# Kernel tuning notes

Hardware: AMD Instinct MI355X
Metric: run time of the kernel (lower is better)

Reference implementation:

```python
import jax, jax.numpy as jnp
import numpy as np

N, E, CIN, H, OUT, L = 100000, 1200000, 3, 64, 3, 3
EPS = 1e-7  # GENConv message epsilon


def setup_inputs() -> dict:
    key = jax.random.key(0)
    ks = jax.random.split(key, 8)
    f = lambda k, s, sc=0.1: (jax.random.normal(k, s, jnp.float32) * sc)
    return {
        "x": f(ks[0], (N, CIN), 1.0),
        "edge_index": jax.random.randint(ks[1], (2, E), 0, N, jnp.int32),
        "enc_W": f(ks[2], (CIN, H)),
        "enc_b": jnp.zeros((H,), jnp.float32),
        "t": jnp.ones((L,), jnp.float32),
        "mlp_W1": f(ks[3], (L, H, 2 * H)),
        "mlp_b1": jnp.zeros((L, 2 * H), jnp.float32),
        "mlp_g": jnp.ones((L, 2 * H), jnp.float32),
        "mlp_beta": jnp.zeros((L, 2 * H), jnp.float32),
        "mlp_W2": f(ks[4], (L, 2 * H, H)),
        "mlp_b2": jnp.zeros((L, H), jnp.float32),
        "ln_g": jnp.ones((L, H), jnp.float32),
        "ln_b": jnp.zeros((L, H), jnp.float32),
        "lin_W": f(ks[5], (H, OUT)),
        "lin_b": jnp.zeros((OUT,), jnp.float32),
    }


def layer_norm(x, g, b, eps=1e-5):
    mu = jnp.mean(x, -1, keepdims=True)
    var = jnp.var(x, -1, keepdims=True)
    return (x - mu) * jax.lax.rsqrt(var + eps) * g + b


def genconv(x, src, dst, t, W1, b1, g, beta, W2, b2):
    # message: relu(x_j) + eps, per edge  [E, H]
    msg = jax.nn.relu(x[src]) + EPS
    # softmax aggregation with temperature t (per-destination, elementwise)
    logits = msg * t
    m = jax.ops.segment_max(logits, dst, num_segments=N)            # [N, H]
    w = jnp.exp(logits - m[dst])                                    # [E, H]
    denom = jax.ops.segment_sum(w, dst, num_segments=N)             # [N, H]
    agg = jax.ops.segment_sum(msg * (w / denom[dst]), dst, num_segments=N)
    # root residual + MLP [H -> 2H -> LN -> ReLU -> H]
    out = agg + x
    h = jax.nn.relu(layer_norm(out @ W1 + b1, g, beta))
    return h @ W2 + b2


def reference(x, edge_index, enc_W, enc_b, t, mlp_W1, mlp_b1, mlp_g, mlp_beta,
              mlp_W2, mlp_b2, ln_g, ln_b, lin_W, lin_b):
    src, dst = edge_index[0], edge_index[1]
    h = x @ enc_W + enc_b
    # layers[0].conv applied directly (DeepGCN 'res+' convention)
    h = genconv(h, src, dst, t[0], mlp_W1[0], mlp_b1[0], mlp_g[0], mlp_beta[0],
                mlp_W2[0], mlp_b2[0])
    for i in range(1, L):
        z = jax.nn.relu(layer_norm(h, ln_g[i], ln_b[i]))
        h = h + genconv(z, src, dst, t[i], mlp_W1[i], mlp_b1[i], mlp_g[i],
                        mlp_beta[i], mlp_W2[i], mlp_b2[i])
    h = jax.nn.relu(layer_norm(h, ln_g[0], ln_b[0]))
    return h @ lin_W + lin_b
```

## Files before the change

### kernel.cpp

```cpp
#include <hip/hip_runtime.h>
#include <hip/hip_bf16.h>
#include <math.h>

#define H 64
#define H2 128
#define EPS_MSG 1e-7f
#define LN_EPS 1e-5f
#define LOG2E 1.4426950408889634f
#define LN2 0.6931471805599453f
#define YSTR 136
#define BSTRIDE 4608
#define OSTRIDE 5376
#define CHUNK 8192

typedef __attribute__((ext_vector_type(8))) short bf16x8;
typedef __attribute__((ext_vector_type(4))) float f32x4;

__device__ __forceinline__ unsigned short f2bf(float f) {
    union { float f; unsigned int i; } x; x.f = f;
    unsigned int r = x.i + 0x7FFF + ((x.i >> 16) & 1);
    return (unsigned short)(r >> 16);
}

__global__ __launch_bounds__(256) void bscat_k(const int* __restrict__ src,
                                               const int* __restrict__ dst,
                                               int* __restrict__ bcnt,
                                               unsigned int* __restrict__ bdata,
                                               int E, int nbuck) {
    __shared__ int h[512], base[512];
    for (int i = threadIdx.x; i < nbuck; i += 256) h[i] = 0;
    __syncthreads();
    int lo = blockIdx.x * CHUNK;
    int hi = lo + CHUNK; if (hi > E) hi = E;
    for (int i = lo + threadIdx.x; i < hi; i += 256)
        atomicAdd(&h[dst[i] >> 8], 1);
    __syncthreads();
    for (int i = threadIdx.x; i < nbuck; i += 256) {
        int c = h[i];
        base[i] = c ? atomicAdd(&bcnt[i], c) : 0;
        h[i] = 0;
    }
    __syncthreads();
    for (int i = lo + threadIdx.x; i < hi; i += 256) {
        int d = dst[i];
        int b = d >> 8;
        int pos = base[b] + atomicAdd(&h[b], 1);
        bdata[(size_t)b * BSTRIDE + pos] = ((unsigned int)src[i] << 8) | (unsigned int)(d & 255);
    }
}

__global__ __launch_bounds__(256) void bsort_k(const unsigned int* __restrict__ bdata,
                                               const int* __restrict__ bcnt,
                                               int* __restrict__ row_beg, int* __restrict__ row_end,
                                               int* __restrict__ srcs_sorted,
                                               int Nn) {
    __shared__ unsigned int stage[BSTRIDE];
    __shared__ int cnt[256], pre[256], ex[256];
    int b = blockIdx.x, tid = threadIdx.x;
    int m = bcnt[b]; if (m > BSTRIDE) m = BSTRIDE;
    size_t lo = (size_t)b * BSTRIDE;
    int oLo = b * OSTRIDE;
    for (int i = tid; i < m; i += 256) stage[i] = bdata[lo + i];
    cnt[tid] = 0;
    __syncthreads();
    for (int i = tid; i < m; i += 256) atomicAdd(&cnt[stage[i] & 255], 1);
    __syncthreads();
    int myc = cnt[tid];
    int pc = (myc + 3) & ~3;
    pre[tid] = pc;
    __syncthreads();
    #pragma unroll
    for (int off = 1; off < 256; off <<= 1) {
        int t = (tid >= off) ? pre[tid - off] : 0;
        __syncthreads();
        pre[tid] += t;
        __syncthreads();
    }
    int pexcl = pre[tid] - pc;
    ex[tid] = pexcl;
    int node = (b << 8) + tid;
    if (node < Nn) {
        row_beg[node] = oLo + pexcl;
        row_end[node] = oLo + pexcl + pc;
    }
    for (int p = myc; p < pc; ++p) srcs_sorted[oLo + pexcl + p] = Nn;
    __syncthreads();
    cnt[tid] = 0;
    __syncthreads();
    for (int i = tid; i < m; i += 256) {
        unsigned int v = stage[i];
        int dl = v & 255;
        int p = ex[dl] + atomicAdd(&cnt[dl], 1);
        srcs_sorted[oLo + p] = (int)(v >> 8);
    }
}

__global__ void wprep_k(const float* __restrict__ W1, const float* __restrict__ W2,
                        unsigned short* __restrict__ Wf1, unsigned short* __restrict__ Wf2) {
    int idx = blockIdx.x * 256 + threadIdx.x;
    const int half = 3 * 8192;
    if (idx < half) {
        int layer = idx / 8192, rem = idx - layer * 8192;
        int t = rem >> 9;
        int l = (rem >> 3) & 63;
        int i = rem & 7;
        int h = t >> 3, ct = t & 7;
        int kpos = h * 32 + (l >> 4) * 8 + i;
        int k = (kpos & 3) * 16 + (kpos >> 2);
        int j = ct * 16 + (l & 15);
        Wf1[idx] = f2bf(W1[(size_t)layer * H * H2 + (size_t)k * H2 + j]);
    } else if (idx < 2 * half) {
        int id2 = idx - half;
        int layer = id2 / 8192, rem = id2 - layer * 8192;
        int t = rem >> 9;
        int l = (rem >> 3) & 63;
        int i = rem & 7;
        int kk = t >> 2, ct2 = t & 3;
        int k = kk * 32 + (l >> 4) * 8 + i;
        int j = ct2 * 16 + (l & 15);
        Wf2[id2] = f2bf(W2[(size_t)layer * H2 * H + (size_t)k * H + j]);
    }
}

__global__ void encoder_k(const float* __restrict__ x, const float* __restrict__ W,
                          const float* __restrict__ b,
                          unsigned short* __restrict__ Zself, unsigned short* __restrict__ Zmsg,
                          const float* __restrict__ t, int Nn) {
    int idx = blockIdx.x * blockDim.x + threadIdx.x;
    if (idx >= (Nn + 1) * H) return;
    int n = idx >> 6, c = idx & 63;
    if (n == Nn) { Zmsg[idx] = f2bf(-200.f); return; }
    float acc = b[c];
    #pragma unroll
    for (int k = 0; k < 3; ++k) acc = fmaf(x[n * 3 + k], W[k * H + c], acc);
    int j = (c & 15) * 4 + (c >> 4);
    Zself[(size_t)n * H + j] = f2bf(acc);
    Zmsg[(size_t)n * H + j]  = f2bf(fmaxf(acc, 0.f) * (LOG2E) * t[0]);
}

__global__ __launch_bounds__(256) void gather_k(
    const unsigned short* __restrict__ Zmsg, const unsigned short* __restrict__ Zself,
    unsigned short* __restrict__ Gbf,
    const int* __restrict__ row_beg, const int* __restrict__ row_end,
    const int* __restrict__ srcs,
    const float* __restrict__ t, int layer, int Nn)
{
    int wid = threadIdx.x >> 6, lane = threadIdx.x & 63;
    int nA = blockIdx.x * 8 + wid * 2;
    if (nA >= Nn) return;
    int nB = nA + 1;
    bool hasB = (nB < Nn);
    int slot = lane >> 4;
    int ch4  = lane & 15;
    float scale = (LN2) * __builtin_amdgcn_rcpf(t[layer]);

    int begA = row_beg[nA];
    int itA  = (row_end[nA] - begA) >> 2;
    int begB = hasB ? row_beg[nB] : begA;
    int itB  = hasB ? (row_end[nB] - begB) >> 2 : 0;
    const int* spA = srcs + begA;
    const int* spB = srcs + begB;

    const unsigned short* selfTab = (layer == 0) ? Zself : Zmsg;
    uint2 svA = *(const uint2*)(selfTab + (size_t)nA * H + ch4 * 4);
    uint2 svB = hasB ? *(const uint2*)(selfTab + (size_t)nB * H + ch4 * 4) : svA;

    #define LQ(qq, sp, i)                                                      \
        {                                                                      \
            int s = sp[4 * (i) + slot];                                        \
            qq = *(const uint2*)(Zmsg + (size_t)s * H + ch4 * 4);              \
        }

    #define PROC(qq, d0, d1, d2, d3, s0, s1, s2, s3)                           \
        {                                                                      \
            float u0 = __uint_as_float(qq.x << 16);                            \
            float u1 = __uint_as_float(qq.x & 0xffff0000u);                    \
            float u2 = __uint_as_float(qq.y << 16);                            \
            float u3 = __uint_as_float(qq.y & 0xffff0000u);                    \
            float w0 = __builtin_amdgcn_exp2f(u0);                             \
            float w1 = __builtin_amdgcn_exp2f(u1);                             \
            float w2 = __builtin_amdgcn_exp2f(u2);                             \
            float w3 = __builtin_amdgcn_exp2f(u3);                             \
            d0 += w0; d1 += w1; d2 += w2; d3 += w3;                            \
            s0 = fmaf(u0, w0, s0); s1 = fmaf(u1, w1, s1);                      \
            s2 = fmaf(u2, w2, s2); s3 = fmaf(u3, w3, s3);                      \
        }
    #define PROCA(qq) PROC(qq, dA0, dA1, dA2, dA3, sA0, sA1, sA2, sA3)
    #define PROCB(qq) PROC(qq, dB0, dB1, dB2, dB3, sB0, sB1, sB2, sB3)

    uint2 a0 = {0,0}, a1 = {0,0}, a2 = {0,0}, a3 = {0,0};
    uint2 b0 = {0,0}, b1 = {0,0}, b2 = {0,0}, b3 = {0,0};
    if (itA > 0) LQ(a0, spA, 0)
    if (itB > 0) LQ(b0, spB, 0)
    if (itA > 1) LQ(a1, spA, 1)
    if (itB > 1) LQ(b1, spB, 1)
    if (itA > 2) LQ(a2, spA, 2)
    if (itB > 2) LQ(b2, spB, 2)
    if (itA > 3) LQ(a3, spA, 3)
    if (itB > 3) LQ(b3, spB, 3)

    float dA0=0.f,dA1=0.f,dA2=0.f,dA3=0.f,sA0=0.f,sA1=0.f,sA2=0.f,sA3=0.f;
    float dB0=0.f,dB1=0.f,dB2=0.f,dB3=0.f,sB0=0.f,sB1=0.f,sB2=0.f,sB3=0.f;

    if (itA > 0) {
        int i = 0;
        #pragma unroll 1
        for (; i + 4 < itA; i += 4) {
            PROCA(a0) LQ(a0, spA, i + 4)
            PROCA(a1) if (i + 5 < itA) LQ(a1, spA, i + 5)
            PROCA(a2) if (i + 6 < itA) LQ(a2, spA, i + 6)
            PROCA(a3) if (i + 7 < itA) LQ(a3, spA, i + 7)
        }
        PROCA(a0)
        if (i + 1 < itA) PROCA(a1)
        if (i + 2 < itA) PROCA(a2)
        if (i + 3 < itA) PROCA(a3)
    }
    if (itB > 0) {
        int i = 0;
        #pragma unroll 1
        for (; i + 4 < itB; i += 4) {
            PROCB(b0) LQ(b0, spB, i + 4)
            PROCB(b1) if (i + 5 < itB) LQ(b1, spB, i + 5)
            PROCB(b2) if (i + 6 < itB) LQ(b2, spB, i + 6)
            PROCB(b3) if (i + 7 < itB) LQ(b3, spB, i + 7)
        }
        PROCB(b0)
        if (i + 1 < itB) PROCB(b1)
        if (i + 2 < itB) PROCB(b2)
        if (i + 3 < itB) PROCB(b3)
    }
    #undef LQ
    #undef PROC
    #undef PROCA
    #undef PROCB

    #pragma unroll
    for (int o = 16; o <= 32; o <<= 1) {
        dA0 += __shfl_xor(dA0, o, 64); dA1 += __shfl_xor(dA1, o, 64);
        dA2 += __shfl_xor(dA2, o, 64); dA3 += __shfl_xor(dA3, o, 64);
        sA0 += __shfl_xor(sA0, o, 64); sA1 += __shfl_xor(sA1, o, 64);
        sA2 += __shfl_xor(sA2, o, 64); sA3 += __shfl_xor(sA3, o, 64);
        dB0 += __shfl_xor(dB0, o, 64); dB1 += __shfl_xor(dB1, o, 64);
        dB2 += __shfl_xor(dB2, o, 64); dB3 += __shfl_xor(dB3, o, 64);
        sB0 += __shfl_xor(sB0, o, 64); sB1 += __shfl_xor(sB1, o, 64);
        sB2 += __shfl_xor(sB2, o, 64); sB3 += __shfl_xor(sB3, o, 64);
    }

    if (slot == 0) {
        {
            float o0 = __uint_as_float(svA.x << 16);
            float o1 = __uint_as_float(svA.x & 0xffff0000u);
            float o2 = __uint_as_float(svA.y << 16);
            float o3 = __uint_as_float(svA.y & 0xffff0000u);
            if (layer != 0) { o0 *= scale; o1 *= scale; o2 *= scale; o3 *= scale; }
            if (itA > 0) {
                o0 += fmaf(sA0 * __builtin_amdgcn_rcpf(dA0), scale, EPS_MSG);
                o1 += fmaf(sA1 * __builtin_amdgcn_rcpf(dA1), scale, EPS_MSG);
                o2 += fmaf(sA2 * __builtin_amdgcn_rcpf(dA2), scale, EPS_MSG);
                o3 += fmaf(sA3 * __builtin_amdgcn_rcpf(dA3), scale, EPS_MSG);
            }
            uint2 pv;
            pv.x = (unsigned int)f2bf(o0) | ((unsigned int)f2bf(o1) << 16);
            pv.y = (unsigned int)f2bf(o2) | ((unsigned int)f2bf(o3) << 16);
            *(uint2*)(Gbf + (size_t)nA * H + ch4 * 4) = pv;
        }
        if (hasB) {
            float o0 = __uint_as_float(svB.x << 16);
            float o1 = __uint_as_float(svB.x & 0xffff0000u);
            float o2 = __uint_as_float(svB.y << 16);
            float o3 = __uint_as_float(svB.y & 0xffff0000u);
            if (layer != 0) { o0 *= scale; o1 *= scale; o2 *= scale; o3 *= scale; }
            if (itB > 0) {
                o0 += fmaf(sB0 * __builtin_amdgcn_rcpf(dB0), scale, EPS_MSG);
                o1 += fmaf(sB1 * __builtin_amdgcn_rcpf(dB1), scale, EPS_MSG);
                o2 += fmaf(sB2 * __builtin_amdgcn_rcpf(dB2), scale, EPS_MSG);
                o3 += fmaf(sB3 * __builtin_amdgcn_rcpf(dB3), scale, EPS_MSG);
            }
            uint2 pv;
            pv.x = (unsigned int)f2bf(o0) | ((unsigned int)f2bf(o1) << 16);
            pv.y = (unsigned int)f2bf(o2) | ((unsigned int)f2bf(o3) << 16);
            *(uint2*)(Gbf + (size_t)nB * H + ch4 * 4) = pv;
        }
    }
}

__global__ __launch_bounds__(256) void mlp_k(
    const unsigned short* __restrict__ Gbf, float* __restrict__ B,
    const unsigned short* __restrict__ Wf1, const unsigned short* __restrict__ Wf2,
    const float* __restrict__ b1, const float* __restrict__ g,
    const float* __restrict__ beta, const float* __restrict__ b2,
    unsigned short* __restrict__ Zmsg,
    const float* __restrict__ tptr, const float* __restrict__ ln_g,
    const float* __restrict__ ln_b, const float* __restrict__ lin_W,
    const float* __restrict__ lin_b, float* __restrict__ outp,
    int wlayer, int lnidx, int resid, int mode, int Nn)
{
    __shared__ __align__(16) unsigned short yt[4][16 * YSTR];
    int wid = threadIdx.x >> 6, lane = threadIdx.x & 63;
    int gq = lane >> 4, c = lane & 15;
    int n0 = (blockIdx.x * 4 + wid) * 16;

    Wf1 += (size_t)wlayer * 8192; Wf2 += (size_t)wlayer * 8192;
    b1 += wlayer * H2; g += wlayer * H2; beta += wlayer * H2; b2 += wlayer * H;

    int nA = n0 + c; if (nA >= Nn) nA = Nn - 1;
    bf16x8 a0 = *(const bf16x8*)(Gbf + (size_t)nA * H + gq * 8);
    bf16x8 a1 = *(const bf16x8*)(Gbf + (size_t)nA * H + 32 + gq * 8);

    f32x4 acc[8];
    #pragma unroll
    for (int ct = 0; ct < 8; ++ct) {
        f32x4 z = {0.f, 0.f, 0.f, 0.f};
        bf16x8 w0 = *(const bf16x8*)(Wf1 + (size_t)(ct * 64 + lane) * 8);
        bf16x8 w1 = *(const bf16x8*)(Wf1 + (size_t)((8 + ct) * 64 + lane) * 8);
        z = __builtin_amdgcn_mfma_f32_16x16x32_bf16(a0, w0, z, 0, 0, 0);
        z = __builtin_amdgcn_mfma_f32_16x16x32_bf16(a1, w1, z, 0, 0, 0);
        acc[ct] = z;
    }

    float v[8][4];
    #pragma unroll
    for (int ct = 0; ct < 8; ++ct) {
        float bias = b1[ct * 16 + c];
        #pragma unroll
        for (int r = 0; r < 4; ++r) v[ct][r] = acc[ct][r] + bias;
    }
    float mean[4], inv[4];
    #pragma unroll
    for (int r = 0; r < 4; ++r) {
        float s = 0.f;
        #pragma unroll
        for (int ct = 0; ct < 8; ++ct) s += v[ct][r];
        #pragma unroll
        for (int o = 1; o < 16; o <<= 1) s += __shfl_xor(s, o, 64);
        mean[r] = s * (1.f / H2);
    }
    #pragma unroll
    for (int r = 0; r < 4; ++r) {
        float s = 0.f;
        #pragma unroll
        for (int ct = 0; ct < 8; ++ct) { float d = v[ct][r] - mean[r]; s = fmaf(d, d, s); }
        #pragma unroll
        for (int o = 1; o < 16; o <<= 1) s += __shfl_xor(s, o, 64);
        inv[r] = rsqrtf(s * (1.f / H2) + LN_EPS);
    }
    unsigned short* Y = yt[wid];
    #pragma unroll
    for (int ct = 0; ct < 8; ++ct) {
        float gg = g[ct * 16 + c], bb = beta[ct * 16 + c];
        #pragma unroll
        for (int r = 0; r < 4; ++r) {
            float yv = fmaxf(fmaf((v[ct][r] - mean[r]) * inv[r], gg, bb), 0.f);
            Y[(gq * 4 + r) * YSTR + ct * 16 + c] = f2bf(yv);
        }
    }

    f32x4 acc2[4];
    #pragma unroll
    for (int t = 0; t < 4; ++t) acc2[t] = (f32x4){0.f, 0.f, 0.f, 0.f};
    #pragma unroll
    for (int kk = 0; kk < 4; ++kk) {
        bf16x8 af = *(const bf16x8*)(Y + c * YSTR + kk * 32 + gq * 8);
        #pragma unroll
        for (int t = 0; t < 4; ++t) {
            bf16x8 wf = *(const bf16x8*)(Wf2 + (size_t)((kk * 4 + t) * 64 + lane) * 8);
            acc2[t] = __builtin_amdgcn_mfma_f32_16x16x32_bf16(af, wf, acc2[t], 0, 0, 0);
        }
    }

    float b2v[4], gg2[4], bb2[4], lw[4][3];
    const float* g64 = ln_g + lnidx * H;
    const float* be64 = ln_b + lnidx * H;
    #pragma unroll
    for (int tt = 0; tt < 4; ++tt) {
        b2v[tt] = b2[tt * 16 + c];
        gg2[tt] = g64[tt * 16 + c];
        bb2[tt] = be64[tt * 16 + c];
    }
    if (mode == 1) {
        #pragma unroll
        for (int tt = 0; tt < 4; ++tt)
            #pragma unroll
            for (int k = 0; k < 3; ++k) lw[tt][k] = lin_W[(tt * 16 + c) * 3 + k];
    }
    float kmsg = (mode == 0) ? (LOG2E * tptr[lnidx]) : 0.f;

    #pragma unroll
    for (int r = 0; r < 4; ++r) {
        int n = n0 + gq * 4 + r;
        int nc = (n < Nn) ? n : (Nn - 1);
        float hv[4];
        #pragma unroll
        for (int tt = 0; tt < 4; ++tt) hv[tt] = acc2[tt][r] + b2v[tt];
        if (resid) {
            float4 old = *(const float4*)&B[(size_t)nc * H + c * 4];
            hv[0] += old.x; hv[1] += old.y; hv[2] += old.z; hv[3] += old.w;
        }
        float s = hv[0] + hv[1] + hv[2] + hv[3];
        #pragma unroll
        for (int o = 1; o < 16; o <<= 1) s += __shfl_xor(s, o, 64);
        float mu = s * (1.f / H);
        float q = 0.f;
        #pragma unroll
        for (int tt = 0; tt < 4; ++tt) { float d = hv[tt] - mu; q = fmaf(d, d, q); }
        #pragma unroll
        for (int o = 1; o < 16; o <<= 1) q += __shfl_xor(q, o, 64);
        float iv = rsqrtf(q * (1.f / H) + LN_EPS);
        float z[4];
        #pragma unroll
        for (int tt = 0; tt < 4; ++tt)
            z[tt] = fmaxf(fmaf((hv[tt] - mu) * iv, gg2[tt], bb2[tt]), 0.f);

        if (mode == 0) {
            if (n < Nn) {
                float4 hq = {hv[0], hv[1], hv[2], hv[3]};
                *(float4*)&B[(size_t)n * H + c * 4] = hq;
                uint2 zm;
                zm.x = (unsigned int)f2bf(z[0] * kmsg) | ((unsigned int)f2bf(z[1] * kmsg) << 16);
                zm.y = (unsigned int)f2bf(z[2] * kmsg) | ((unsigned int)f2bf(z[3] * kmsg) << 16);
                *(uint2*)&Zmsg[(size_t)n * H + c * 4] = zm;
            }
        } else {
            float p0 = 0.f, p1 = 0.f, p2 = 0.f;
            #pragma unroll
            for (int tt = 0; tt < 4; ++tt) {
                p0 = fmaf(z[tt], lw[tt][0], p0);
                p1 = fmaf(z[tt], lw[tt][1], p1);
                p2 = fmaf(z[tt], lw[tt][2], p2);
            }
            #pragma unroll
            for (int o = 1; o < 16; o <<= 1) {
                p0 += __shfl_xor(p0, o, 64);
                p1 += __shfl_xor(p1, o, 64);
                p2 += __shfl_xor(p2, o, 64);
            }
            if (c == 0 && n < Nn) {
                outp[(size_t)n * 3 + 0] = p0 + lin_b[0];
                outp[(size_t)n * 3 + 1] = p1 + lin_b[1];
                outp[(size_t)n * 3 + 2] = p2 + lin_b[2];
            }
        }
    }
}

extern "C" void kernel_launch(void* const* d_in, const int* in_sizes, int n_in,
                              void* d_out, int out_size, void* d_ws, size_t ws_size,
                              hipStream_t stream) {
    const float* x        = (const float*)d_in[0];
    const int*   eidx     = (const int*)  d_in[1];
    const float* enc_W    = (const float*)d_in[2];
    const float* enc_b    = (const float*)d_in[3];
    const float* t        = (const float*)d_in[4];
    const float* mlp_W1   = (const float*)d_in[5];
    const float* mlp_b1   = (const float*)d_in[6];
    const float* mlp_g    = (const float*)d_in[7];
    const float* mlp_beta = (const float*)d_in[8];
    const float* mlp_W2   = (const float*)d_in[9];
    const float* mlp_b2   = (const float*)d_in[10];
    const float* ln_g     = (const float*)d_in[11];
    const float* ln_b     = (const float*)d_in[12];
    const float* lin_W    = (const float*)d_in[13];
    const float* lin_b    = (const float*)d_in[14];
    float* out = (float*)d_out;

    const int N = in_sizes[0] / 3;
    const int E = in_sizes[1] / 2;
    const int* src = eidx;
    const int* dst = eidx + E;
    const int nbuck = (N + 255) >> 8;

    float* Bm = (float*)d_ws;
    int* row_beg   = (int*)(Bm + (size_t)N * H);
    int* row_end   = row_beg + N;
    int* bcnt      = row_end + N;
    int* srcs_sorted = bcnt + 512;
    unsigned short* Zself = (unsigned short*)(srcs_sorted + 512 * OSTRIDE);
    unsigned short* Zmsg  = Zself + (size_t)N * H;
    unsigned short* Gbf   = Zmsg + (size_t)(N + 1) * H;
    unsigned short* Wf1   = Gbf + (size_t)N * H;
    unsigned short* Wf2   = Wf1 + 3 * 8192;
    unsigned int* bdata = (unsigned int*)Gbf;

    const int eBlocks = (E + CHUNK - 1) / CHUNK;

    hipMemsetAsync(bcnt, 0, 512 * sizeof(int), stream);
    bscat_k<<<eBlocks, 256, 0, stream>>>(src, dst, bcnt, bdata, E, nbuck);
    bsort_k<<<nbuck, 256, 0, stream>>>(bdata, bcnt, row_beg, row_end, srcs_sorted, N);

    wprep_k<<<192, 256, 0, stream>>>(mlp_W1, mlp_W2, Wf1, Wf2);
    encoder_k<<<((size_t)(N + 1) * H + 255) / 256, 256, 0, stream>>>(x, enc_W, enc_b, Zself, Zmsg, t, N);

    const int gBlocks   = (N + 7) / 8;
    const int mlpBlocks = (N + 63) / 64;

    gather_k<<<gBlocks, 256, 0, stream>>>(Zmsg, Zself, Gbf, row_beg, row_end, srcs_sorted, t, 0, N);
    mlp_k<<<mlpBlocks, 256, 0, stream>>>(Gbf, Bm, Wf1, Wf2, mlp_b1, mlp_g, mlp_beta, mlp_b2,
                                         Zmsg, t, ln_g, ln_b, lin_W, lin_b, out,
                                         0, 1, 0, 0, N);
    gather_k<<<gBlocks, 256, 0, stream>>>(Zmsg, Zself, Gbf, row_beg, row_end, srcs_sorted, t, 1, N);
    mlp_k<<<mlpBlocks, 256, 0, stream>>>(Gbf, Bm, Wf1, Wf2, mlp_b1, mlp_g, mlp_beta, mlp_b2,
                                         Zmsg, t, ln_g, ln_b, lin_W, lin_b, out,
                                         1, 2, 1, 0, N);
    gather_k<<<gBlocks, 256, 0, stream>>>(Zmsg, Zself, Gbf, row_beg, row_end, srcs_sorted, t, 2, N);
    mlp_k<<<mlpBlocks, 256, 0, stream>>>(Gbf, Bm, Wf1, Wf2, mlp_b1, mlp_g, mlp_beta, mlp_b2,
                                         Zmsg, t, ln_g, ln_b, lin_W, lin_b, out,
                                         2, 0, 1, 1, N);
}
```

Baseline: 339.7 us.

## Gather four nodes per wavefront with packed row descriptors and lane-parallel epilogue

The gather kernel now handles four destination nodes per wavefront instead of two, keeping 16 outstanding neighbour loads in flight. Row start and quad count are packed into one int2 array written by bsort, so each wave reads its row metadata with two 16-byte loads. The epilogue is spread across all four lane slots, so each slot writes one node rather than only slot 0 writing. The cost is higher register pressure from four sets of accumulators, plus sequential per-node loops that can leave lanes idle when degrees differ.

```diff
diff --git a/kernel.cpp b/kernel.cpp
--- a/kernel.cpp
+++ b/kernel.cpp
@@ -51,7 +51,7 @@
 
 __global__ __launch_bounds__(256) void bsort_k(const unsigned int* __restrict__ bdata,
                                                const int* __restrict__ bcnt,
-                                               int* __restrict__ row_beg, int* __restrict__ row_end,
+                                               int2* __restrict__ rowq,
                                                int* __restrict__ srcs_sorted,
                                                int Nn) {
     __shared__ unsigned int stage[BSTRIDE];
@@ -79,10 +79,8 @@
     int pexcl = pre[tid] - pc;
     ex[tid] = pexcl;
     int node = (b << 8) + tid;
-    if (node < Nn) {
-        row_beg[node] = oLo + pexcl;
-        row_end[node] = oLo + pexcl + pc;
-    }
+    if (node < Nn) rowq[node] = make_int2(oLo + pexcl, pc >> 2);
+    else           rowq[node] = make_int2(0, 0);
     for (int p = myc; p < pc; ++p) srcs_sorted[oLo + pexcl + p] = Nn;
     __syncthreads();
     cnt[tid] = 0;
@@ -141,37 +139,59 @@
 __global__ __launch_bounds__(256) void gather_k(
     const unsigned short* __restrict__ Zmsg, const unsigned short* __restrict__ Zself,
     unsigned short* __restrict__ Gbf,
-    const int* __restrict__ row_beg, const int* __restrict__ row_end,
+    const int2* __restrict__ rowq,
     const int* __restrict__ srcs,
     const float* __restrict__ t, int layer, int Nn)
 {
     int wid = threadIdx.x >> 6, lane = threadIdx.x & 63;
-    int nA = blockIdx.x * 8 + wid * 2;
+    int nA = (blockIdx.x * 4 + wid) * 4;
     if (nA >= Nn) return;
-    int nB = nA + 1;
-    bool hasB = (nB < Nn);
     int slot = lane >> 4;
     int ch4  = lane & 15;
     float scale = (LN2) * __builtin_amdgcn_rcpf(t[layer]);
 
-    int begA = row_beg[nA];
-    int itA  = (row_end[nA] - begA) >> 2;
-    int begB = hasB ? row_beg[nB] : begA;
-    int itB  = hasB ? (row_end[nB] - begB) >> 2 : 0;
-    const int* spA = srcs + begA;
-    const int* spB = srcs + begB;
-
+    int4 rAB = *(const int4*)&rowq[nA];
+    int4 rCD = *(const int4*)&rowq[nA + 2];
+    int begA = rAB.x, qA = rAB.y, begB = rAB.z, qB = rAB.w;
+    int begC = rCD.x, qC = rCD.y, begD = rCD.z, qD = rCD.w;
+
+    int ns = nA + slot; if (ns >= Nn) ns = Nn - 1;
     const unsigned short* selfTab = (layer == 0) ? Zself : Zmsg;
-    uint2 svA = *(const uint2*)(selfTab + (size_t)nA * H + ch4 * 4);
-    uint2 svB = hasB ? *(const uint2*)(selfTab + (size_t)nB * H + ch4 * 4) : svA;
-
-    #define LQ(qq, sp, i)                                                      \
+    uint2 sv = *(const uint2*)(selfTab + (size_t)ns * H + ch4 * 4);
+
+    #define LQ(qq, beg, i)                                                     \
         {                                                                      \
-            int s = sp[4 * (i) + slot];                                        \
+            int s = srcs[(beg) + 4 * (i) + slot];                              \
             qq = *(const uint2*)(Zmsg + (size_t)s * H + ch4 * 4);              \
         }
 
-    #define PROC(qq, d0, d1, d2, d3, s0, s1, s2, s3)                           \
+    uint2 a0={0,0},a1={0,0},a2={0,0},a3={0,0};
+    uint2 b0={0,0},b1={0,0},b2={0,0},b3={0,0};
+    uint2 c0={0,0},c1={0,0},c2={0,0},c3={0,0};
+    uint2 e0={0,0},e1={0,0},e2={0,0},e3={0,0};
+    if (qA > 0) LQ(a0, begA, 0)
+    if (qB > 0) LQ(b0, begB, 0)
+    if (qC > 0) LQ(c0, begC, 0)
+    if (qD > 0) LQ(e0, begD, 0)
+    if (qA > 1) LQ(a1, begA, 1)
+    if (qB > 1) LQ(b1, begB, 1)
+    if (qC > 1) LQ(c1, begC, 1)
+    if (qD > 1) LQ(e1, begD, 1)
+    if (qA > 2) LQ(a2, begA, 2)
+    if (qB > 2) LQ(b2, begB, 2)
+    if (qC > 2) LQ(c2, begC, 2)
+    if (qD > 2) LQ(e2, begD, 2)
+    if (qA > 3) LQ(a3, begA, 3)
+    if (qB > 3) LQ(b3, begB, 3)
+    if (qC > 3) LQ(c3, begC, 3)
+    if (qD > 3) LQ(e3, begD, 3)
+
+    float dA0=0.f,dA1=0.f,dA2=0.f,dA3=0.f,sA0=0.f,sA1=0.f,sA2=0.f,sA3=0.f;
+    float dB0=0.f,dB1=0.f,dB2=0.f,dB3=0.f,sB0=0.f,sB1=0.f,sB2=0.f,sB3=0.f;
+    float dC0=0.f,dC1=0.f,dC2=0.f,dC3=0.f,sC0=0.f,sC1=0.f,sC2=0.f,sC3=0.f;
+    float dD0=0.f,dD1=0.f,dD2=0.f,dD3=0.f,sD0=0.f,sD1=0.f,sD2=0.f,sD3=0.f;
+
+    #define PROC(qq, dd0,dd1,dd2,dd3, ss0,ss1,ss2,ss3)                         \
         {                                                                      \
             float u0 = __uint_as_float(qq.x << 16);                            \
             float u1 = __uint_as_float(qq.x & 0xffff0000u);                    \
@@ -181,59 +201,77 @@
             float w1 = __builtin_amdgcn_exp2f(u1);                             \
             float w2 = __builtin_amdgcn_exp2f(u2);                             \
             float w3 = __builtin_amdgcn_exp2f(u3);                             \
-            d0 += w0; d1 += w1; d2 += w2; d3 += w3;                            \
-            s0 = fmaf(u0, w0, s0); s1 = fmaf(u1, w1, s1);                      \
-            s2 = fmaf(u2, w2, s2); s3 = fmaf(u3, w3, s3);                      \
-        }
-    #define PROCA(qq) PROC(qq, dA0, dA1, dA2, dA3, sA0, sA1, sA2, sA3)
-    #define PROCB(qq) PROC(qq, dB0, dB1, dB2, dB3, sB0, sB1, sB2, sB3)
-
-    uint2 a0 = {0,0}, a1 = {0,0}, a2 = {0,0}, a3 = {0,0};
-    uint2 b0 = {0,0}, b1 = {0,0}, b2 = {0,0}, b3 = {0,0};
-    if (itA > 0) LQ(a0, spA, 0)
-    if (itB > 0) LQ(b0, spB, 0)
-    if (itA > 1) LQ(a1, spA, 1)
-    if (itB > 1) LQ(b1, spB, 1)
-    if (itA > 2) LQ(a2, spA, 2)
-    if (itB > 2) LQ(b2, spB, 2)
-    if (itA > 3) LQ(a3, spA, 3)
-    if (itB > 3) LQ(b3, spB, 3)
-
-    float dA0=0.f,dA1=0.f,dA2=0.f,dA3=0.f,sA0=0.f,sA1=0.f,sA2=0.f,sA3=0.f;
-    float dB0=0.f,dB1=0.f,dB2=0.f,dB3=0.f,sB0=0.f,sB1=0.f,sB2=0.f,sB3=0.f;
-
-    if (itA > 0) {
+            dd0 += w0; dd1 += w1; dd2 += w2; dd3 += w3;                        \
+            ss0 = fmaf(u0, w0, ss0); ss1 = fmaf(u1, w1, ss1);                  \
+            ss2 = fmaf(u2, w2, ss2); ss3 = fmaf(u3, w3, ss3);                  \
+        }
+    #define PROCA(qq) PROC(qq, dA0,dA1,dA2,dA3, sA0,sA1,sA2,sA3)
+    #define PROCB(qq) PROC(qq, dB0,dB1,dB2,dB3, sB0,sB1,sB2,sB3)
+    #define PROCC(qq) PROC(qq, dC0,dC1,dC2,dC3, sC0,sC1,sC2,sC3)
+    #define PROCD(qq) PROC(qq, dD0,dD1,dD2,dD3, sD0,sD1,sD2,sD3)
+
+    if (qA > 0) {
         int i = 0;
         #pragma unroll 1
-        for (; i + 4 < itA; i += 4) {
-            PROCA(a0) LQ(a0, spA, i + 4)
-            PROCA(a1) if (i + 5 < itA) LQ(a1, spA, i + 5)
-            PROCA(a2) if (i + 6 < itA) LQ(a2, spA, i + 6)
-            PROCA(a3) if (i + 7 < itA) LQ(a3, spA, i + 7)
+        for (; i + 4 < qA; i += 4) {
+            PROCA(a0) LQ(a0, begA, i + 4)
+            PROCA(a1) if (i + 5 < qA) LQ(a1, begA, i + 5)
+            PROCA(a2) if (i + 6 < qA) LQ(a2, begA, i + 6)
+            PROCA(a3) if (i + 7 < qA) LQ(a3, begA, i + 7)
         }
         PROCA(a0)
-        if (i + 1 < itA) PROCA(a1)
-        if (i + 2 < itA) PROCA(a2)
-        if (i + 3 < itA) PROCA(a3)
-    }
-    if (itB > 0) {
+        if (i + 1 < qA) PROCA(a1)
+        if (i + 2 < qA) PROCA(a2)
+        if (i + 3 < qA) PROCA(a3)
+    }
+    if (qB > 0) {
         int i = 0;
         #pragma unroll 1
-        for (; i + 4 < itB; i += 4) {
-            PROCB(b0) LQ(b0, spB, i + 4)
-            PROCB(b1) if (i + 5 < itB) LQ(b1, spB, i + 5)
-            PROCB(b2) if (i + 6 < itB) LQ(b2, spB, i + 6)
-            PROCB(b3) if (i + 7 < itB) LQ(b3, spB, i + 7)
+        for (; i + 4 < qB; i += 4) {
+            PROCB(b0) LQ(b0, begB, i + 4)
+            PROCB(b1) if (i + 5 < qB) LQ(b1, begB, i + 5)
+            PROCB(b2) if (i + 6 < qB) LQ(b2, begB, i + 6)
+            PROCB(b3) if (i + 7 < qB) LQ(b3, begB, i + 7)
         }
         PROCB(b0)
-        if (i + 1 < itB) PROCB(b1)
-        if (i + 2 < itB) PROCB(b2)
-        if (i + 3 < itB) PROCB(b3)
+        if (i + 1 < qB) PROCB(b1)
+        if (i + 2 < qB) PROCB(b2)
+        if (i + 3 < qB) PROCB(b3)
+    }
+    if (qC > 0) {
+        int i = 0;
+        #pragma unroll 1
+        for (; i + 4 < qC; i += 4) {
+            PROCC(c0) LQ(c0, begC, i + 4)
+            PROCC(c1) if (i + 5 < qC) LQ(c1, begC, i + 5)
+            PROCC(c2) if (i + 6 < qC) LQ(c2, begC, i + 6)
+            PROCC(c3) if (i + 7 < qC) LQ(c3, begC, i + 7)
+        }
+        PROCC(c0)
+        if (i + 1 < qC) PROCC(c1)
+        if (i + 2 < qC) PROCC(c2)
+        if (i + 3 < qC) PROCC(c3)
+    }
+    if (qD > 0) {
+        int i = 0;
+        #pragma unroll 1
+        for (; i + 4 < qD; i += 4) {
+            PROCD(e0) LQ(e0, begD, i + 4)
+            PROCD(e1) if (i + 5 < qD) LQ(e1, begD, i + 5)
+            PROCD(e2) if (i + 6 < qD) LQ(e2, begD, i + 6)
+            PROCD(e3) if (i + 7 < qD) LQ(e3, begD, i + 7)
+        }
+        PROCD(e0)
+        if (i + 1 < qD) PROCD(e1)
+        if (i + 2 < qD) PROCD(e2)
+        if (i + 3 < qD) PROCD(e3)
     }
     #undef LQ
     #undef PROC
     #undef PROCA
     #undef PROCB
+    #undef PROCC
+    #undef PROCD
 
     #pragma unroll
     for (int o = 16; o <= 32; o <<= 1) {
@@ -245,44 +283,43 @@
         dB2 += __shfl_xor(dB2, o, 64); dB3 += __shfl_xor(dB3, o, 64);
         sB0 += __shfl_xor(sB0, o, 64); sB1 += __shfl_xor(sB1, o, 64);
         sB2 += __shfl_xor(sB2, o, 64); sB3 += __shfl_xor(sB3, o, 64);
-    }
-
-    if (slot == 0) {
-        {
-            float o0 = __uint_as_float(svA.x << 16);
-            float o1 = __uint_as_float(svA.x & 0xffff0000u);
-            float o2 = __uint_as_float(svA.y << 16);
-            float o3 = __uint_as_float(svA.y & 0xffff0000u);
-            if (layer != 0) { o0 *= scale; o1 *= scale; o2 *= scale; o3 *= scale; }
-            if (itA > 0) {
-                o0 += fmaf(sA0 * __builtin_amdgcn_rcpf(dA0), scale, EPS_MSG);
-                o1 += fmaf(sA1 * __builtin_amdgcn_rcpf(dA1), scale, EPS_MSG);
-                o2 += fmaf(sA2 * __builtin_amdgcn_rcpf(dA2), scale, EPS_MSG);
-                o3 += fmaf(sA3 * __builtin_amdgcn_rcpf(dA3), scale, EPS_MSG);
-            }
-            uint2 pv;
-            pv.x = (unsigned int)f2bf(o0) | ((unsigned int)f2bf(o1) << 16);
-            pv.y = (unsigned int)f2bf(o2) | ((unsigned int)f2bf(o3) << 16);
-            *(uint2*)(Gbf + (size_t)nA * H + ch4 * 4) = pv;
-        }
-        if (hasB) {
-            float o0 = __uint_as_float(svB.x << 16);
-            float o1 = __uint_as_float(svB.x & 0xffff0000u);
-            float o2 = __uint_as_float(svB.y << 16);
-            float o3 = __uint_as_float(svB.y & 0xffff0000u);
-            if (layer != 0) { o0 *= scale; o1 *= scale; o2 *= scale; o3 *= scale; }
-            if (itB > 0) {
-                o0 += fmaf(sB0 * __builtin_amdgcn_rcpf(dB0), scale, EPS_MSG);
-                o1 += fmaf(sB1 * __builtin_amdgcn_rcpf(dB1), scale, EPS_MSG);
-                o2 += fmaf(sB2 * __builtin_amdgcn_rcpf(dB2), scale, EPS_MSG);
-                o3 += fmaf(sB3 * __builtin_amdgcn_rcpf(dB3), scale, EPS_MSG);
-            }
-            uint2 pv;
-            pv.x = (unsigned int)f2bf(o0) | ((unsigned int)f2bf(o1) << 16);
-            pv.y = (unsigned int)f2bf(o2) | ((unsigned int)f2bf(o3) << 16);
-            *(uint2*)(Gbf + (size_t)nB * H + ch4 * 4) = pv;
-        }
-    }
+        dC0 += __shfl_xor(dC0, o, 64); dC1 += __shfl_xor(dC1, o, 64);
+        dC2 += __shfl_xor(dC2, o, 64); dC3 += __shfl_xor(dC3, o, 64);
+        sC0 += __shfl_xor(sC0, o, 64); sC1 += __shfl_xor(sC1, o, 64);
+        sC2 += __shfl_xor(sC2, o, 64); sC3 += __shfl_xor(sC3, o, 64);
+        dD0 += __shfl_xor(dD0, o, 64); dD1 += __shfl_xor(dD1, o, 64);
+        dD2 += __shfl_xor(dD2, o, 64); dD3 += __shfl_xor(dD3, o, 64);
+        sD0 += __shfl_xor(sD0, o, 64); sD1 += __shfl_xor(sD1, o, 64);
+        sD2 += __shfl_xor(sD2, o, 64); sD3 += __shfl_xor(sD3, o, 64);
+    }
+
+    #define SEL(vA, vB, vC, vD) ((slot & 2) ? ((slot & 1) ? (vD) : (vC)) : ((slot & 1) ? (vB) : (vA)))
+    float ds0 = SEL(dA0, dB0, dC0, dD0), ds1 = SEL(dA1, dB1, dC1, dD1);
+    float ds2 = SEL(dA2, dB2, dC2, dD2), ds3 = SEL(dA3, dB3, dC3, dD3);
+    float ss0 = SEL(sA0, sB0, sC0, sD0), ss1 = SEL(sA1, sB1, sC1, sD1);
+    float ss2 = SEL(sA2, sB2, sC2, sD2), ss3 = SEL(sA3, sB3, sC3, sD3);
+    int   qn  = SEL(qA, qB, qC, qD);
+    #undef SEL
+
+    float o0 = __uint_as_float(sv.x << 16);
+    float o1 = __uint_as_float(sv.x & 0xffff0000u);
+    float o2 = __uint_as_float(sv.y << 16);
+    float o3 = __uint_as_float(sv.y & 0xffff0000u);
+    if (layer != 0) { o0 *= scale; o1 *= scale; o2 *= scale; o3 *= scale; }
+    float t0 = fmaf(ss0 * __builtin_amdgcn_rcpf(ds0), scale, EPS_MSG);
+    float t1 = fmaf(ss1 * __builtin_amdgcn_rcpf(ds1), scale, EPS_MSG);
+    float t2 = fmaf(ss2 * __builtin_amdgcn_rcpf(ds2), scale, EPS_MSG);
+    float t3 = fmaf(ss3 * __builtin_amdgcn_rcpf(ds3), scale, EPS_MSG);
+    o0 += (qn > 0) ? t0 : 0.f;
+    o1 += (qn > 0) ? t1 : 0.f;
+    o2 += (qn > 0) ? t2 : 0.f;
+    o3 += (qn > 0) ? t3 : 0.f;
+
+    uint2 pv;
+    pv.x = (unsigned int)f2bf(o0) | ((unsigned int)f2bf(o1) << 16);
+    pv.y = (unsigned int)f2bf(o2) | ((unsigned int)f2bf(o3) << 16);
+    if (nA + slot < Nn)
+        *(uint2*)(Gbf + (size_t)(nA + slot) * H + ch4 * 4) = pv;
 }
 
 __global__ __launch_bounds__(256) void mlp_k(
@@ -471,9 +508,8 @@
     const int nbuck = (N + 255) >> 8;
 
     float* Bm = (float*)d_ws;
-    int* row_beg   = (int*)(Bm + (size_t)N * H);
-    int* row_end   = row_beg + N;
-    int* bcnt      = row_end + N;
+    int2* rowq = (int2*)(Bm + (size_t)N * H);
+    int* bcnt      = (int*)(rowq + 512 * 256);
     int* srcs_sorted = bcnt + 512;
     unsigned short* Zself = (unsigned short*)(srcs_sorted + 512 * OSTRIDE);
     unsigned short* Zmsg  = Zself + (size_t)N * H;
@@ -486,23 +522,23 @@
 
     hipMemsetAsync(bcnt, 0, 512 * sizeof(int), stream);
     bscat_k<<<eBlocks, 256, 0, stream>>>(src, dst, bcnt, bdata, E, nbuck);
-    bsort_k<<<nbuck, 256, 0, stream>>>(bdata, bcnt, row_beg, row_end, srcs_sorted, N);
+    bsort_k<<<nbuck, 256, 0, stream>>>(bdata, bcnt, rowq, srcs_sorted, N);
 
     wprep_k<<<192, 256, 0, stream>>>(mlp_W1, mlp_W2, Wf1, Wf2);
     encoder_k<<<((size_t)(N + 1) * H + 255) / 256, 256, 0, stream>>>(x, enc_W, enc_b, Zself, Zmsg, t, N);
 
-    const int gBlocks   = (N + 7) / 8;
+    const int gBlocks   = (N + 15) / 16;
     const int mlpBlocks = (N + 63) / 64;
 
-    gather_k<<<gBlocks, 256, 0, stream>>>(Zmsg, Zself, Gbf, row_beg, row_end, srcs_sorted, t, 0, N);
+    gather_k<<<gBlocks, 256, 0, stream>>>(Zmsg, Zself, Gbf, rowq, srcs_sorted, t, 0, N);
     mlp_k<<<mlpBlocks, 256, 0, stream>>>(Gbf, Bm, Wf1, Wf2, mlp_b1, mlp_g, mlp_beta, mlp_b2,
                                          Zmsg, t, ln_g, ln_b, lin_W, lin_b, out,
                                          0, 1, 0, 0, N);
-    gather_k<<<gBlocks, 256, 0, stream>>>(Zmsg, Zself, Gbf, row_beg, row_end, srcs_sorted, t, 1, N);
+    gather_k<<<gBlocks, 256, 0, stream>>>(Zmsg, Zself, Gbf, rowq, srcs_sorted, t, 1, N);
     mlp_k<<<mlpBlocks, 256, 0, stream>>>(Gbf, Bm, Wf1, Wf2, mlp_b1, mlp_g, mlp_beta, mlp_b2,
                                          Zmsg, t, ln_g, ln_b, lin_W, lin_b, out,
                                          1, 2, 1, 0, N);
-    gather_k<<<gBlocks, 256, 0, stream>>>(Zmsg, Zself, Gbf, row_beg, row_end, srcs_sorted, t, 2, N);
+    gather_k<<<gBlocks, 256, 0, stream>>>(Zmsg, Zself, Gbf, rowq, srcs_sorted, t, 2, N);
     mlp_k<<<mlpBlocks, 256, 0, stream>>>(Gbf, Bm, Wf1, Wf2, mlp_b1, mlp_g, mlp_beta, mlp_b2,
                                          Zmsg, t, ln_g, ln_b, lin_W, lin_b, out,
                                          2, 0, 1, 1, N);
```

After: 351.2 us. +3.4%, slower.
